# Performance work log

Hardware: AMD Instinct MI355X
Metric: run time of the kernel (lower is better)

The kernel has to match this reference:

```python
import jax, jax.numpy as jnp
import numpy as np

N_NODES = 100000
N_EDGES = 1600000
IN_DIM, HID, OUT = 128, 64, 64
KERNEL = 5
PAD = (KERNEL - 1) // 2


def setup_inputs() -> dict:
    key = jax.random.key(0)
    ks = jax.random.split(key, 12)
    s = lambda fan_in: 1.0 / np.sqrt(fan_in)
    return {
        "x": jax.random.normal(ks[0], (N_NODES, IN_DIM), jnp.float32),
        "edge_index": jax.random.randint(ks[1], (2, N_EDGES), 0, N_NODES, jnp.int32),
        "W0": jax.random.normal(ks[2], (IN_DIM, HID), jnp.float32) * s(IN_DIM),
        "b0": jnp.zeros((HID,), jnp.float32),
        "W1": jax.random.normal(ks[3], (HID, HID), jnp.float32) * s(HID),
        "b1": jnp.zeros((HID,), jnp.float32),
        "W2": jax.random.normal(ks[4], (HID, OUT), jnp.float32) * s(HID),
        "b2": jnp.zeros((OUT,), jnp.float32),
        "Wp": jax.random.normal(ks[5], (OUT, 1), jnp.float32) * s(OUT),
        "bp": jnp.zeros((1,), jnp.float32),
        "conv1_w": jax.random.normal(ks[6], (OUT, OUT, KERNEL), jnp.float32) * s(OUT * KERNEL),
        "conv1_b": jnp.zeros((OUT,), jnp.float32),
        "conv2_w": jax.random.normal(ks[7], (OUT, OUT, KERNEL), jnp.float32) * s(OUT * KERNEL),
        "conv2_b": jnp.zeros((OUT,), jnp.float32),
        "lin_w": jax.random.normal(ks[8], (2 * OUT, OUT), jnp.float32) * s(2 * OUT),
        "lin_b": jnp.zeros((OUT,), jnp.float32),
    }


def gcn_conv(h, W, b, src, dst, n):
    """PyG GCNConv: x @ W, add self-loops, D^-1/2 (A+I) D^-1/2 aggregation, + bias."""
    h = h @ W  # [N, out]
    loop = jnp.arange(n, dtype=src.dtype)
    srcl = jnp.concatenate([src, loop])
    dstl = jnp.concatenate([dst, loop])
    deg = jax.ops.segment_sum(jnp.ones_like(dstl, dtype=h.dtype), dstl, num_segments=n)
    dinv = jnp.where(deg > 0, jax.lax.rsqrt(deg), 0.0)
    norm = dinv[srcl] * dinv[dstl]  # [E+N]
    out = jax.ops.segment_sum(h[srcl] * norm[:, None], dstl, num_segments=n)
    return out + b


def conv1d(x, w, b):
    # x: [1, C, N], w: [Cout, Cin, K]
    y = jax.lax.conv_general_dilated(x, w, window_strides=(1,), padding=[(PAD, PAD)],
                                     dimension_numbers=("NCH", "OIH", "NCH"))
    return y + b[None, :, None]


def reference(x, edge_index, W0, b0, W1, b1, W2, b2, Wp, bp,
              conv1_w, conv1_b, conv2_w, conv2_b, lin_w, lin_b):
    n = x.shape[0]
    src, dst = edge_index[0], edge_index[1]
    # eval mode: dropout layers are identity
    h = jax.nn.relu(gcn_conv(x, W0, b0, src, dst, n))
    h = jax.nn.relu(gcn_conv(h, W1, b1, src, dst, n))
    h1 = gcn_conv(h, W2, b2, src, dst, n)  # [N, OUT]
    g_score = h1 @ Wp + bp  # [N, 1]
    sorted_idx = jnp.argsort(g_score[:, 0])  # ascending, as torch.sort
    inverse_idx = jnp.argsort(sorted_idx)
    sorted_x = g_score[sorted_idx] * h1[sorted_idx]  # [N, OUT]
    sorted_x = sorted_x.T[None]  # [1, OUT, N]
    sorted_x = jax.nn.relu(conv1d(sorted_x, conv1_w, conv1_b))
    sorted_x = conv1d(sorted_x, conv2_w, conv2_b)
    sorted_x = sorted_x[0].T  # [N, OUT]
    h2 = sorted_x[inverse_idx]  # un-sort back to node order
    out = jnp.concatenate([h1, h2], axis=1) @ lin_w + lin_b  # [N, OUT]
    return out
```

## Files before the change

kernel.cpp:

```cpp
#include <hip/hip_runtime.h>

#define NN 100000
#define NE 1600000
#define SORT_M 131072
#define NB_SCAN 98
#define TS 8192

__global__ void zero_counts(int* c) {
    int i = blockIdx.x * blockDim.x + threadIdx.x;
    if (i < NN) c[i] = 0;
}

__global__ void count_dst(const int* __restrict__ dst, int* c) {
    int e = blockIdx.x * blockDim.x + threadIdx.x;
    if (e < NE) atomicAdd(&c[dst[e]], 1);
}

__global__ void scan_p1(const int* __restrict__ c, int* __restrict__ bsums) {
    __shared__ int red[256];
    int b = blockIdx.x, t = threadIdx.x;
    int s = 0;
    for (int i = t; i < 1024; i += 256) {
        int idx = b * 1024 + i;
        s += (idx < NN) ? c[idx] : 0;
    }
    red[t] = s; __syncthreads();
    for (int o = 128; o; o >>= 1) {
        if (t < o) red[t] += red[t + o];
        __syncthreads();
    }
    if (t == 0) bsums[b] = red[0];
}

__global__ void scan_p2(int* bsums) {
    __shared__ int tmp[128];
    int t = threadIdx.x;
    int v = (t < NB_SCAN) ? bsums[t] : 0;
    tmp[t] = v; __syncthreads();
    for (int o = 1; o < 128; o <<= 1) {
        int add = (t >= o) ? tmp[t - o] : 0;
        __syncthreads();
        tmp[t] += add;
        __syncthreads();
    }
    if (t < NB_SCAN) bsums[t] = tmp[t] - v;
}

__global__ void scan_p3(const int* __restrict__ c, const int* __restrict__ bsums,
                        int* __restrict__ offs, int* __restrict__ cursor,
                        float* __restrict__ dinv) {
    __shared__ int thr[256];
    int b = blockIdx.x, t = threadIdx.x;
    int base = b * 1024 + t * 4;
    int cv[4];
#pragma unroll
    for (int j = 0; j < 4; j++) cv[j] = (base + j < NN) ? c[base + j] : 0;
    int s = cv[0] + cv[1] + cv[2] + cv[3];
    thr[t] = s; __syncthreads();
    for (int o = 1; o < 256; o <<= 1) {
        int add = (t >= o) ? thr[t - o] : 0;
        __syncthreads();
        thr[t] += add;
        __syncthreads();
    }
    int ex = thr[t] - s + bsums[b];
#pragma unroll
    for (int j = 0; j < 4; j++) {
        if (base + j < NN) {
            offs[base + j] = ex;
            cursor[base + j] = ex;
            dinv[base + j] = rsqrtf((float)(cv[j] + 1));
            ex += cv[j];
        }
    }
}

__global__ void csr_scatter_p(const int* __restrict__ src, const int* __restrict__ dst,
                              int* cursor, int* __restrict__ csr, int pass) {
    int e = blockIdx.x * blockDim.x + threadIdx.x;
    if (e >= NE) return;
    int d = dst[e];
    if ((d >> 15) != pass) return;
    int p = atomicAdd(&cursor[d], 1);
    csr[p] = src[e];
}

__device__ inline void swz_w(const float* __restrict__ W, float4* __restrict__ o, int idx) {
    int k4 = idx >> 6, co = idx & 63;
    o[idx] = make_float4(W[(4 * k4 + 0) * 64 + co], W[(4 * k4 + 1) * 64 + co],
                         W[(4 * k4 + 2) * 64 + co], W[(4 * k4 + 3) * 64 + co]);
}

__device__ inline void swz_c(const float* __restrict__ w, float4* __restrict__ o, int idx) {
    int co = idx & 63, j = (idx >> 6) & 15, k = idx >> 10;
    int b = co * 320 + k;
    o[idx] = make_float4(w[b + (4 * j + 0) * 5], w[b + (4 * j + 1) * 5],
                         w[b + (4 * j + 2) * 5], w[b + (4 * j + 3) * 5]);
}

__global__ void swizzle_all(const float* W0, const float* W1, const float* W2,
                            const float* lw, const float* c1w, const float* c2w,
                            float4* w0sw, float4* w1sw, float4* w2sw,
                            float4* linsw, float4* c1sw, float4* c2sw) {
    int idx = blockIdx.x * blockDim.x + threadIdx.x;
    if (idx < 2048)        swz_w(W0, w0sw, idx);
    else if (idx < 3072)   swz_w(W1, w1sw, idx - 2048);
    else if (idx < 4096)   swz_w(W2, w2sw, idx - 3072);
    else if (idx < 6144)   swz_w(lw, linsw, idx - 4096);
    else if (idx < 11264)  swz_c(c1w, c1sw, idx - 6144);
    else if (idx < 16384)  swz_c(c2w, c2sw, idx - 11264);
}

template <int K, bool RELU>
__global__ __launch_bounds__(256) void gemm64r(const float* __restrict__ X,
                                               const float4* __restrict__ Wsw,
                                               const float* __restrict__ dinv,
                                               float* __restrict__ Y, int n) {
    constexpr int KV = K / 4;
    constexpr int SH = (KV == 32) ? 5 : 4;
    __shared__ float4 xs[64][KV];
    int tid = threadIdx.x;
    int r0 = blockIdx.x * 64;
    for (int idx = tid; idx < 64 * KV; idx += 256) {
        int r = idx >> SH, k4 = idx & (KV - 1);
        int row = r0 + r;
        float4 v = make_float4(0.f, 0.f, 0.f, 0.f);
        if (row < n) v = *reinterpret_cast<const float4*>(X + (size_t)row * K + 4 * k4);
        if (RELU) {
            v.x = fmaxf(v.x, 0.f); v.y = fmaxf(v.y, 0.f);
            v.z = fmaxf(v.z, 0.f); v.w = fmaxf(v.w, 0.f);
        }
        xs[r][k4] = v;
    }
    __syncthreads();
    int co2 = tid & 31, rg = tid >> 5;
    int c0 = 2 * co2;
    float acc0[8], acc1[8];
#pragma unroll
    for (int i = 0; i < 8; i++) { acc0[i] = 0.f; acc1[i] = 0.f; }
    for (int k4 = 0; k4 < KV; k4++) {
        float4 wa = Wsw[k4 * 64 + c0];
        float4 wb = Wsw[k4 * 64 + c0 + 1];
#pragma unroll
        for (int i = 0; i < 8; i++) {
            float4 xv = xs[rg * 8 + i][k4];
            acc0[i] += xv.x * wa.x + xv.y * wa.y + xv.z * wa.z + xv.w * wa.w;
            acc1[i] += xv.x * wb.x + xv.y * wb.y + xv.z * wb.z + xv.w * wb.w;
        }
    }
#pragma unroll
    for (int i = 0; i < 8; i++) {
        int row = r0 + rg * 8 + i;
        if (row < n) {
            float dv = dinv[row];
            *reinterpret_cast<float2*>(Y + (size_t)row * 64 + c0) =
                make_float2(acc0[i] * dv, acc1[i] * dv);
        }
    }
}

template <int SCORE>
__global__ __launch_bounds__(256) void agg_pull(const float* __restrict__ H,
                                                const int* __restrict__ offs,
                                                const int* __restrict__ counts,
                                                const int* __restrict__ csr,
                                                const float* __restrict__ dinv,
                                                const float* __restrict__ bias,
                                                float* __restrict__ Y,
                                                const float* __restrict__ Wp,
                                                const float* __restrict__ bp,
                                                float* __restrict__ sc,
                                                unsigned* __restrict__ keys,
                                                int* __restrict__ vals) {
    int lane = threadIdx.x & 63;
    int node = blockIdx.x * 4 + (threadIdx.x >> 6);
    if (node >= NN) return;
    float dv = dinv[node];
    float acc = H[(size_t)node * 64 + lane];
    int off = offs[node], cnt = counts[node];
    int i = 0;
    for (; i + 7 < cnt; i += 8) {
        int p0 = csr[off + i];
        int p1 = csr[off + i + 1];
        int p2 = csr[off + i + 2];
        int p3 = csr[off + i + 3];
        int p4 = csr[off + i + 4];
        int p5 = csr[off + i + 5];
        int p6 = csr[off + i + 6];
        int p7 = csr[off + i + 7];
        float h0 = H[(size_t)p0 * 64 + lane];
        float h1 = H[(size_t)p1 * 64 + lane];
        float h2 = H[(size_t)p2 * 64 + lane];
        float h3 = H[(size_t)p3 * 64 + lane];
        float h4 = H[(size_t)p4 * 64 + lane];
        float h5 = H[(size_t)p5 * 64 + lane];
        float h6 = H[(size_t)p6 * 64 + lane];
        float h7 = H[(size_t)p7 * 64 + lane];
        acc += ((h0 + h1) + (h2 + h3)) + ((h4 + h5) + (h6 + h7));
    }
    for (; i < cnt; i++) {
        acc += H[(size_t)csr[off + i] * 64 + lane];
    }
    float o = acc * dv + bias[lane];
    Y[(size_t)node * 64 + lane] = o;
    if (SCORE) {
        float v = o * Wp[lane];
        for (int of = 32; of; of >>= 1) v += __shfl_down(v, of, 64);
        if (lane == 0) {
            float s = v + bp[0];
            sc[node] = s;
            unsigned u = __float_as_uint(s);
            u = (u & 0x80000000u) ? ~u : (u | 0x80000000u);
            keys[node] = u;
            vals[node] = node;
        }
    }
}

__global__ __launch_bounds__(1024) void bitonic_local_sort8k(unsigned* key, int* val) {
    __shared__ unsigned sk[TS];
    __shared__ int sv[TS];
    int t = threadIdx.x;
    int base = blockIdx.x * TS;
    for (int i = t; i < TS; i += 1024) {
        if (base + i < NN) { sk[i] = key[base + i]; sv[i] = val[base + i]; }
        else               { sk[i] = 0xFFFFFFFFu;  sv[i] = 0x7FFFFFFF; }
    }
    for (int k = 2; k <= TS; k <<= 1) {
        for (int j = k >> 1; j > 0; j >>= 1) {
            __syncthreads();
            for (int c = t; c < TS / 2; c += 1024) {
                int i = 2 * c - (c & (j - 1));
                bool up = (((base + i) & k) == 0);
                unsigned a = sk[i], b = sk[i + j];
                if ((a > b) == up) {
                    sk[i] = b; sk[i + j] = a;
                    int tv = sv[i]; sv[i] = sv[i + j]; sv[i + j] = tv;
                }
            }
        }
    }
    __syncthreads();
    for (int i = t; i < TS; i += 1024) { key[base + i] = sk[i]; val[base + i] = sv[i]; }
}

__global__ void bitonic_global(unsigned* key, int* val, int j, int k) {
    int i = blockIdx.x * blockDim.x + threadIdx.x;
    int ixj = i ^ j;
    if (ixj > i) {
        bool up = ((i & k) == 0);
        unsigned a = key[i], b = key[ixj];
        if ((a > b) == up) {
            key[i] = b; key[ixj] = a;
            int tv = val[i]; val[i] = val[ixj]; val[ixj] = tv;
        }
    }
}

__global__ __launch_bounds__(1024) void bitonic_local_merge8k(unsigned* key, int* val, int k) {
    __shared__ unsigned sk[TS];
    __shared__ int sv[TS];
    int t = threadIdx.x;
    int base = blockIdx.x * TS;
    for (int i = t; i < TS; i += 1024) { sk[i] = key[base + i]; sv[i] = val[base + i]; }
    for (int j = TS / 2; j > 0; j >>= 1) {
        __syncthreads();
        for (int c = t; c < TS / 2; c += 1024) {
            int i = 2 * c - (c & (j - 1));
            bool up = (((base + i) & k) == 0);
            unsigned a = sk[i], b = sk[i + j];
            if ((a > b) == up) {
                sk[i] = b; sk[i + j] = a;
                int tv = sv[i]; sv[i] = sv[i + j]; sv[i + j] = tv;
            }
        }
    }
    __syncthreads();
    for (int i = t; i < TS; i += 1024) { key[base + i] = sk[i]; val[base + i] = sv[i]; }
}

template <bool GATHER>
__global__ __launch_bounds__(256) void conv1d_k(const float* __restrict__ X,
                                                const int* __restrict__ vals,
                                                const float* __restrict__ sc,
                                                const float4* __restrict__ cw,
                                                const float* __restrict__ bias,
                                                float* __restrict__ Y, int relu,
                                                int* __restrict__ inv) {
    __shared__ float4 xs[68][16];
    int tid = threadIdx.x;
    int r0 = blockIdx.x * 64;
    for (int idx = tid; idx < 68 * 16; idx += 256) {
        int r = idx >> 4, k4 = idx & 15;
        int row = r0 + r - 2;
        float4 v = make_float4(0.f, 0.f, 0.f, 0.f);
        if (row >= 0 && row < NN) {
            if (GATHER) {
                int vs = vals[row];
                float s = sc[vs];
                v = *reinterpret_cast<const float4*>(X + (size_t)vs * 64 + 4 * k4);
                v.x *= s; v.y *= s; v.z *= s; v.w *= s;
                if (k4 == 0) inv[vs] = row;
            } else {
                v = *reinterpret_cast<const float4*>(X + (size_t)row * 64 + 4 * k4);
            }
        }
        xs[r][k4] = v;
    }
    __syncthreads();
    int co2 = tid & 31, rg = tid >> 5;
    int c0 = 2 * co2;
    float acc0[8], acc1[8];
#pragma unroll
    for (int i = 0; i < 8; i++) { acc0[i] = 0.f; acc1[i] = 0.f; }
    for (int j = 0; j < 16; j++) {
        float4 xv[12];
#pragma unroll
        for (int t2 = 0; t2 < 12; t2++) xv[t2] = xs[rg * 8 + t2][j];
#pragma unroll
        for (int k = 0; k < 5; k++) {
            float4 wa = cw[(k * 16 + j) * 64 + c0];
            float4 wb = cw[(k * 16 + j) * 64 + c0 + 1];
#pragma unroll
            for (int i = 0; i < 8; i++) {
                float4 x4 = xv[i + k];
                acc0[i] += x4.x * wa.x + x4.y * wa.y + x4.z * wa.z + x4.w * wa.w;
                acc1[i] += x4.x * wb.x + x4.y * wb.y + x4.z * wb.z + x4.w * wb.w;
            }
        }
    }
    float b0v = bias[c0], b1v = bias[c0 + 1];
#pragma unroll
    for (int i = 0; i < 8; i++) {
        int row = r0 + rg * 8 + i;
        if (row < NN) {
            float o0 = acc0[i] + b0v, o1 = acc1[i] + b1v;
            if (relu) { o0 = fmaxf(o0, 0.f); o1 = fmaxf(o1, 0.f); }
            *reinterpret_cast<float2*>(Y + (size_t)row * 64 + c0) = make_float2(o0, o1);
        }
    }
}

__global__ __launch_bounds__(256) void final_k(const float* __restrict__ C,
                                               const float* __restrict__ H2,
                                               const int* __restrict__ inv,
                                               const float4* __restrict__ linsw,
                                               const float* __restrict__ lb,
                                               float* __restrict__ Yout) {
    __shared__ float4 xs[64][32];
    int tid = threadIdx.x;
    int r0 = blockIdx.x * 64;
    for (int idx = tid; idx < 64 * 32; idx += 256) {
        int r = idx >> 5, k4 = idx & 31;
        int row = r0 + r;
        float4 v = make_float4(0.f, 0.f, 0.f, 0.f);
        if (row < NN) {
            if (k4 < 16) v = *reinterpret_cast<const float4*>(C + (size_t)row * 64 + 4 * k4);
            else v = *reinterpret_cast<const float4*>(H2 + (size_t)inv[row] * 64 + 4 * (k4 - 16));
        }
        xs[r][k4] = v;
    }
    __syncthreads();
    int co2 = tid & 31, rg = tid >> 5;
    int c0 = 2 * co2;
    float acc0[8], acc1[8];
#pragma unroll
    for (int i = 0; i < 8; i++) { acc0[i] = 0.f; acc1[i] = 0.f; }
    for (int k4 = 0; k4 < 32; k4++) {
        float4 wa = linsw[k4 * 64 + c0];
        float4 wb = linsw[k4 * 64 + c0 + 1];
#pragma unroll
        for (int i = 0; i < 8; i++) {
            float4 xv = xs[rg * 8 + i][k4];
            acc0[i] += xv.x * wa.x + xv.y * wa.y + xv.z * wa.z + xv.w * wa.w;
            acc1[i] += xv.x * wb.x + xv.y * wb.y + xv.z * wb.z + xv.w * wb.w;
        }
    }
    float b0v = lb[c0], b1v = lb[c0 + 1];
#pragma unroll
    for (int i = 0; i < 8; i++) {
        int row = r0 + rg * 8 + i;
        if (row < NN)
            *reinterpret_cast<float2*>(Yout + (size_t)row * 64 + c0) =
                make_float2(acc0[i] + b0v, acc1[i] + b1v);
    }
}

extern "C" void kernel_launch(void* const* d_in, const int* in_sizes, int n_in,
                              void* d_out, int out_size, void* d_ws, size_t ws_size,
                              hipStream_t stream) {
    const float* x   = (const float*)d_in[0];
    const int*   ei  = (const int*)d_in[1];
    const float* W0  = (const float*)d_in[2];
    const float* b0  = (const float*)d_in[3];
    const float* W1  = (const float*)d_in[4];
    const float* b1  = (const float*)d_in[5];
    const float* W2  = (const float*)d_in[6];
    const float* b2  = (const float*)d_in[7];
    const float* Wp  = (const float*)d_in[8];
    const float* bp  = (const float*)d_in[9];
    const float* c1w = (const float*)d_in[10];
    const float* c1b = (const float*)d_in[11];
    const float* c2w = (const float*)d_in[12];
    const float* c2b = (const float*)d_in[13];
    const float* lw  = (const float*)d_in[14];
    const float* lb  = (const float*)d_in[15];
    const int* src = ei;
    const int* dst = ei + NE;

    float* A     = (float*)d_ws;
    float* B     = A + (size_t)NN * 64;
    float* dinv  = B + (size_t)NN * 64;
    float* score = dinv + NN;
    unsigned* keys = (unsigned*)(score + NN);
    int* vals    = (int*)(keys + SORT_M);
    int* inv     = vals + SORT_M;
    int* counts  = inv + NN;
    int* offs    = counts + NN;
    int* cursor  = offs + NN;
    int* bsums   = cursor + NN;
    int* csr     = bsums + 128;
    float4* w0sw  = (float4*)(csr + NE);
    float4* w1sw  = w0sw + 2048;
    float4* w2sw  = w1sw + 1024;
    float4* linsw = w2sw + 1024;
    float4* c1sw  = linsw + 2048;
    float4* c2sw  = c1sw + 5120;
    float* Cb = (float*)d_out;

    const int GR64 = (NN + 63) / 64;
    const int GN4 = (NN + 3) / 4;
    const int GE = (NE + 255) / 256;

    zero_counts<<<(NN + 255) / 256, 256, 0, stream>>>(counts);
    count_dst<<<GE, 256, 0, stream>>>(dst, counts);
    scan_p1<<<NB_SCAN, 256, 0, stream>>>(counts, bsums);
    scan_p2<<<1, 128, 0, stream>>>(bsums);
    scan_p3<<<NB_SCAN, 256, 0, stream>>>(counts, bsums, offs, cursor, dinv);
    for (int pass = 0; pass < 4; pass++)
        csr_scatter_p<<<GE, 256, 0, stream>>>(src, dst, cursor, csr, pass);

    swizzle_all<<<64, 256, 0, stream>>>(W0, W1, W2, lw, c1w, c2w,
                                        w0sw, w1sw, w2sw, linsw, c1sw, c2sw);

    gemm64r<128, false><<<GR64, 256, 0, stream>>>(x, w0sw, dinv, A, NN);
    agg_pull<0><<<GN4, 256, 0, stream>>>(A, offs, counts, csr, dinv, b0, B,
                                         nullptr, nullptr, nullptr, nullptr, nullptr);
    gemm64r<64, true><<<GR64, 256, 0, stream>>>(B, w1sw, dinv, A, NN);
    agg_pull<0><<<GN4, 256, 0, stream>>>(A, offs, counts, csr, dinv, b1, B,
                                         nullptr, nullptr, nullptr, nullptr, nullptr);
    gemm64r<64, true><<<GR64, 256, 0, stream>>>(B, w2sw, dinv, A, NN);
    agg_pull<1><<<GN4, 256, 0, stream>>>(A, offs, counts, csr, dinv, b2, Cb,
                                         Wp, bp, score, keys, vals);

    bitonic_local_sort8k<<<SORT_M / TS, 1024, 0, stream>>>(keys, vals);
    for (int k = 2 * TS; k <= SORT_M; k <<= 1) {
        for (int j = k >> 1; j >= TS; j >>= 1)
            bitonic_global<<<SORT_M / 256, 256, 0, stream>>>(keys, vals, j, k);
        bitonic_local_merge8k<<<SORT_M / TS, 1024, 0, stream>>>(keys, vals, k);
    }

    conv1d_k<true><<<GR64, 256, 0, stream>>>(Cb, vals, score, c1sw, c1b, B, 1, inv);
    conv1d_k<false><<<GR64, 256, 0, stream>>>(B, nullptr, nullptr, c2sw, c2b, A, 0, nullptr);

    final_k<<<GR64, 256, 0, stream>>>(Cb, A, inv, linsw, lb, (float*)d_out);
}
```

Before: 972.8 us.

## Replace bitonic sort with 4-pass LSD radix sort and single-pass CSR scatter

Swaps the multi-launch bitonic sort over a padded 131072-element array for a stable 8-bit LSD radix sort in four passes. Each pass runs a histogram, a single-block scan and a ballot-based stable scatter, with ping-pong key/value buffers. The four-pass dst-partitioned CSR scatter is also collapsed into one launch, giving up whatever atomic locality the partitioning provided. Radix sorting does O(n) work per pass instead of O(n log^2 n), and its stability matches the argsort tie order.

After: 924.0 us. 5.0% less time.

```diff
diff --git a/kernel.cpp b/kernel.cpp
--- a/kernel.cpp
+++ b/kernel.cpp
@@ -2,9 +2,10 @@
 
 #define NN 100000
 #define NE 1600000
-#define SORT_M 131072
 #define NB_SCAN 98
-#define TS 8192
+#define RBLK 98
+#define NENT (256 * RBLK)
+#define RSEG 25
 
 __global__ void zero_counts(int* c) {
     int i = blockIdx.x * blockDim.x + threadIdx.x;
@@ -75,13 +76,11 @@
     }
 }
 
-__global__ void csr_scatter_p(const int* __restrict__ src, const int* __restrict__ dst,
-                              int* cursor, int* __restrict__ csr, int pass) {
+__global__ void csr_scatter(const int* __restrict__ src, const int* __restrict__ dst,
+                            int* cursor, int* __restrict__ csr) {
     int e = blockIdx.x * blockDim.x + threadIdx.x;
     if (e >= NE) return;
-    int d = dst[e];
-    if ((d >> 15) != pass) return;
-    int p = atomicAdd(&cursor[d], 1);
+    int p = atomicAdd(&cursor[dst[e]], 1);
     csr[p] = src[e];
 }
 
@@ -217,66 +216,100 @@
     }
 }
 
-__global__ __launch_bounds__(1024) void bitonic_local_sort8k(unsigned* key, int* val) {
-    __shared__ unsigned sk[TS];
-    __shared__ int sv[TS];
+__global__ __launch_bounds__(256) void radix_hist(const unsigned* __restrict__ keys,
+                                                  int* __restrict__ hist, int shift) {
+    __shared__ int h[256];
     int t = threadIdx.x;
-    int base = blockIdx.x * TS;
-    for (int i = t; i < TS; i += 1024) {
-        if (base + i < NN) { sk[i] = key[base + i]; sv[i] = val[base + i]; }
-        else               { sk[i] = 0xFFFFFFFFu;  sv[i] = 0x7FFFFFFF; }
-    }
-    for (int k = 2; k <= TS; k <<= 1) {
-        for (int j = k >> 1; j > 0; j >>= 1) {
-            __syncthreads();
-            for (int c = t; c < TS / 2; c += 1024) {
-                int i = 2 * c - (c & (j - 1));
-                bool up = (((base + i) & k) == 0);
-                unsigned a = sk[i], b = sk[i + j];
-                if ((a > b) == up) {
-                    sk[i] = b; sk[i + j] = a;
-                    int tv = sv[i]; sv[i] = sv[i + j]; sv[i + j] = tv;
-                }
-            }
-        }
-    }
-    __syncthreads();
-    for (int i = t; i < TS; i += 1024) { key[base + i] = sk[i]; val[base + i] = sv[i]; }
-}
-
-__global__ void bitonic_global(unsigned* key, int* val, int j, int k) {
-    int i = blockIdx.x * blockDim.x + threadIdx.x;
-    int ixj = i ^ j;
-    if (ixj > i) {
-        bool up = ((i & k) == 0);
-        unsigned a = key[i], b = key[ixj];
-        if ((a > b) == up) {
-            key[i] = b; key[ixj] = a;
-            int tv = val[i]; val[i] = val[ixj]; val[ixj] = tv;
-        }
-    }
-}
-
-__global__ __launch_bounds__(1024) void bitonic_local_merge8k(unsigned* key, int* val, int k) {
-    __shared__ unsigned sk[TS];
-    __shared__ int sv[TS];
+    h[t] = 0;
+    __syncthreads();
+    int base = blockIdx.x * 1024;
+    for (int i = t; i < 1024; i += 256) {
+        int idx = base + i;
+        if (idx < NN) atomicAdd(&h[(keys[idx] >> shift) & 255], 1);
+    }
+    __syncthreads();
+    hist[t * RBLK + blockIdx.x] = h[t];
+}
+
+__global__ __launch_bounds__(1024) void radix_scan(int* hist) {
+    __shared__ int partial[1024];
     int t = threadIdx.x;
-    int base = blockIdx.x * TS;
-    for (int i = t; i < TS; i += 1024) { sk[i] = key[base + i]; sv[i] = val[base + i]; }
-    for (int j = TS / 2; j > 0; j >>= 1) {
-        __syncthreads();
-        for (int c = t; c < TS / 2; c += 1024) {
-            int i = 2 * c - (c & (j - 1));
-            bool up = (((base + i) & k) == 0);
-            unsigned a = sk[i], b = sk[i + j];
-            if ((a > b) == up) {
-                sk[i] = b; sk[i + j] = a;
-                int tv = sv[i]; sv[i] = sv[i + j]; sv[i + j] = tv;
-            }
-        }
-    }
-    __syncthreads();
-    for (int i = t; i < TS; i += 1024) { key[base + i] = sk[i]; val[base + i] = sv[i]; }
+    int base = t * RSEG;
+    int loc[RSEG];
+    int s = 0;
+#pragma unroll
+    for (int i = 0; i < RSEG; i++) {
+        int idx = base + i;
+        int v = (idx < NENT) ? hist[idx] : 0;
+        loc[i] = s;
+        s += v;
+    }
+    partial[t] = s;
+    __syncthreads();
+    for (int o = 1; o < 1024; o <<= 1) {
+        int add = (t >= o) ? partial[t - o] : 0;
+        __syncthreads();
+        partial[t] += add;
+        __syncthreads();
+    }
+    int ex = partial[t] - s;
+#pragma unroll
+    for (int i = 0; i < RSEG; i++) {
+        int idx = base + i;
+        if (idx < NENT) hist[idx] = ex + loc[i];
+    }
+}
+
+__global__ __launch_bounds__(256) void radix_scatter(const unsigned* __restrict__ keys_in,
+                                                     const int* __restrict__ vals_in,
+                                                     const int* __restrict__ hist,
+                                                     unsigned* __restrict__ keys_out,
+                                                     int* __restrict__ vals_out, int shift) {
+    __shared__ int cursor[256];
+    __shared__ int whist[4][256];
+    __shared__ int wbase[4][256];
+    int t = threadIdx.x, w = t >> 6, lane = t & 63;
+    cursor[t] = hist[t * RBLK + blockIdx.x];
+    __syncthreads();
+    int base = blockIdx.x * 1024;
+    for (int r = 0; r < 4; r++) {
+        int idx = base + r * 256 + t;
+        bool active = idx < NN;
+        unsigned key = 0;
+        int val = 0, d = -1;
+        if (active) {
+            key = keys_in[idx];
+            val = vals_in[idx];
+            d = (key >> shift) & 255;
+        }
+#pragma unroll
+        for (int q = 0; q < 4; q++) whist[q][t] = 0;
+        __syncthreads();
+        unsigned long long m = __ballot(active);
+#pragma unroll
+        for (int b = 0; b < 8; b++) {
+            unsigned long long bb = __ballot(active && ((d >> b) & 1));
+            m &= ((d >> b) & 1) ? bb : ~bb;
+        }
+        unsigned long long below = ((unsigned long long)1 << lane) - 1;
+        int rank_in_wave = __popcll(m & below);
+        int cnt_in_wave = __popcll(m);
+        if (active && rank_in_wave == 0) whist[w][d] = cnt_in_wave;
+        __syncthreads();
+        int c0 = whist[0][t], c1 = whist[1][t], c2 = whist[2][t], c3 = whist[3][t];
+        wbase[0][t] = 0;
+        wbase[1][t] = c0;
+        wbase[2][t] = c0 + c1;
+        wbase[3][t] = c0 + c1 + c2;
+        __syncthreads();
+        if (active) {
+            int pos = cursor[d] + wbase[w][d] + rank_in_wave;
+            keys_out[pos] = key;
+            vals_out[pos] = val;
+        }
+        __syncthreads();
+        cursor[t] += c0 + c1 + c2 + c3;
+    }
 }
 
 template <bool GATHER>
@@ -408,17 +441,21 @@
     const int* src = ei;
     const int* dst = ei + NE;
 
+    const int NNP = 100352;
     float* A     = (float*)d_ws;
     float* B     = A + (size_t)NN * 64;
     float* dinv  = B + (size_t)NN * 64;
-    float* score = dinv + NN;
-    unsigned* keys = (unsigned*)(score + NN);
-    int* vals    = (int*)(keys + SORT_M);
-    int* inv     = vals + SORT_M;
-    int* counts  = inv + NN;
-    int* offs    = counts + NN;
-    int* cursor  = offs + NN;
-    int* bsums   = cursor + NN;
+    float* score = dinv + NNP;
+    unsigned* keys0 = (unsigned*)(score + NNP);
+    int* vals0   = (int*)(keys0 + NNP);
+    unsigned* keys1 = (unsigned*)(vals0 + NNP);
+    int* vals1   = (int*)(keys1 + NNP);
+    int* rhist   = vals1 + NNP;
+    int* inv     = rhist + NENT;
+    int* counts  = inv + NNP;
+    int* offs    = counts + NNP;
+    int* cursor  = offs + NNP;
+    int* bsums   = cursor + NNP;
     int* csr     = bsums + 128;
     float4* w0sw  = (float4*)(csr + NE);
     float4* w1sw  = w0sw + 2048;
@@ -437,8 +474,7 @@
     scan_p1<<<NB_SCAN, 256, 0, stream>>>(counts, bsums);
     scan_p2<<<1, 128, 0, stream>>>(bsums);
     scan_p3<<<NB_SCAN, 256, 0, stream>>>(counts, bsums, offs, cursor, dinv);
-    for (int pass = 0; pass < 4; pass++)
-        csr_scatter_p<<<GE, 256, 0, stream>>>(src, dst, cursor, csr, pass);
+    csr_scatter<<<GE, 256, 0, stream>>>(src, dst, cursor, csr);
 
     swizzle_all<<<64, 256, 0, stream>>>(W0, W1, W2, lw, c1w, c2w,
                                         w0sw, w1sw, w2sw, linsw, c1sw, c2sw);
@@ -451,16 +487,22 @@
                                          nullptr, nullptr, nullptr, nullptr, nullptr);
     gemm64r<64, true><<<GR64, 256, 0, stream>>>(B, w2sw, dinv, A, NN);
     agg_pull<1><<<GN4, 256, 0, stream>>>(A, offs, counts, csr, dinv, b2, Cb,
-                                         Wp, bp, score, keys, vals);
-
-    bitonic_local_sort8k<<<SORT_M / TS, 1024, 0, stream>>>(keys, vals);
-    for (int k = 2 * TS; k <= SORT_M; k <<= 1) {
-        for (int j = k >> 1; j >= TS; j >>= 1)
-            bitonic_global<<<SORT_M / 256, 256, 0, stream>>>(keys, vals, j, k);
-        bitonic_local_merge8k<<<SORT_M / TS, 1024, 0, stream>>>(keys, vals, k);
-    }
-
-    conv1d_k<true><<<GR64, 256, 0, stream>>>(Cb, vals, score, c1sw, c1b, B, 1, inv);
+                                         Wp, bp, score, keys0, vals0);
+
+    radix_hist<<<RBLK, 256, 0, stream>>>(keys0, rhist, 0);
+    radix_scan<<<1, 1024, 0, stream>>>(rhist);
+    radix_scatter<<<RBLK, 256, 0, stream>>>(keys0, vals0, rhist, keys1, vals1, 0);
+    radix_hist<<<RBLK, 256, 0, stream>>>(keys1, rhist, 8);
+    radix_scan<<<1, 1024, 0, stream>>>(rhist);
+    radix_scatter<<<RBLK, 256, 0, stream>>>(keys1, vals1, rhist, keys0, vals0, 8);
+    radix_hist<<<RBLK, 256, 0, stream>>>(keys0, rhist, 16);
+    radix_scan<<<1, 1024, 0, stream>>>(rhist);
+    radix_scatter<<<RBLK, 256, 0, stream>>>(keys0, vals0, rhist, keys1, vals1, 16);
+    radix_hist<<<RBLK, 256, 0, stream>>>(keys1, rhist, 24);
+    radix_scan<<<1, 1024, 0, stream>>>(rhist);
+    radix_scatter<<<RBLK, 256, 0, stream>>>(keys1, vals1, rhist, keys0, vals0, 24);
+
+    conv1d_k<true><<<GR64, 256, 0, stream>>>(Cb, vals0, score, c1sw, c1b, B, 1, inv);
     conv1d_k<false><<<GR64, 256, 0, stream>>>(B, nullptr, nullptr, c2sw, c2b, A, 0, nullptr);
 
     final_k<<<GR64, 256, 0, stream>>>(Cb, A, inv, linsw, lb, (float*)d_out);
```
